# Kernel optimization log

Measured on AMD Instinct MI355X. Metric: run time of the kernel, lower is better.

## Reference

```python
import jax, jax.numpy as jnp
import numpy as np

N_VARS = 1_000_000
NB, NS, NL = 400_000, 300_000, 200_000  # binary / small-int / large-int counts
C_CLS = 16
N_CON = 500_000
E = 16_000_000
LP_SOL_COL = 8
BIAS_COL = 1
LAMBDA_MEAN, LAMBDA_MAX = 1.0, 0.1


def setup_inputs() -> dict:
    key = jax.random.key(0)
    ks = jax.random.split(key, 10)
    # disjoint variable index partitions: [0,NB) bin, [NB,NB+NS) small int,
    # [NB+NS,NB+NS+NL) large int, rest continuous (var_types==0)
    idx_bin = jnp.arange(NB, dtype=jnp.int64)
    idx_int_small = jnp.arange(NB, NB + NS, dtype=jnp.int64)
    idx_int_large = jnp.arange(NB + NS, NB + NS + NL, dtype=jnp.int64)
    var_types = jnp.concatenate([
        jnp.ones(NB, dtype=jnp.int64),                 # binary
        jnp.full((NS + NL,), 2, dtype=jnp.int64),      # integer
        jnp.zeros(N_VARS - NB - NS - NL, dtype=jnp.int64),  # continuous
    ])
    edge_indices = jnp.stack([
        jax.random.randint(ks[0], (E,), 0, N_CON, dtype=jnp.int64),
        jax.random.randint(ks[1], (E,), 0, N_VARS, dtype=jnp.int64),
    ])
    return {
        'prob_bin': jax.random.uniform(ks[2], (NB, 1), jnp.float32),
        'logits_int_small': jax.random.normal(ks[3], (NS, C_CLS), jnp.float32),
        'int_small_offsets': jax.random.normal(ks[4], (NS,), jnp.float32),
        'pred_int_large': jax.random.normal(ks[5], (NL, 1), jnp.float32),
        'edge_features': jax.random.normal(ks[6], (E, 1), jnp.float32),
        'constraint_features': jax.random.normal(ks[7], (N_CON, 8), jnp.float32),
        'variable_features': jax.random.normal(ks[8], (N_VARS, 16), jnp.float32),
        'idx_bin': idx_bin,
        'idx_int_small': idx_int_small,
        'idx_int_large': idx_int_large,
        'var_types': var_types,
        'edge_indices': edge_indices,
        'n_vars': N_VARS,
    }


def _build_x(prob_bin, logits_int_small, int_small_offsets, pred_int_large,
             variable_features, idx_bin, idx_int_small, idx_int_large,
             var_types, n_vars):
    x = jnp.zeros((n_vars,), dtype=prob_bin.dtype)
    x = x.at[idx_bin].set(prob_bin[:, 0])
    # expected value of small-int class distribution
    probs = jax.nn.softmax(logits_int_small, axis=-1)                  # [NS, C]
    class_values = jnp.arange(logits_int_small.shape[1], dtype=probs.dtype)
    expected = probs @ class_values + int_small_offsets                # [NS]
    x = x.at[idx_int_small].set(expected)
    x = x.at[idx_int_large].set(pred_int_large[:, 0])
    # continuous vars take detached LP solution values
    lp_vals = jax.lax.stop_gradient(variable_features[:, LP_SOL_COL])
    x = jnp.where(var_types == 0, lp_vals, x)
    return x


def reference(prob_bin, logits_int_small, int_small_offsets, pred_int_large,
              edge_features, constraint_features, variable_features,
              idx_bin, idx_int_small, idx_int_large, var_types,
              edge_indices, n_vars):
    x = _build_x(prob_bin, logits_int_small, int_small_offsets, pred_int_large,
                 variable_features, idx_bin, idx_int_small, idx_int_large,
                 var_types, n_vars)
    n_cons = constraint_features.shape[0]
    # sparse A @ x: gather variable values along edges, scale, scatter-add per constraint
    weighted = edge_features.reshape(-1) * x[edge_indices[1]]          # [E]
    Ax = jax.ops.segment_sum(weighted, edge_indices[0], num_segments=n_cons)
    violation = jax.nn.relu(Ax - constraint_features[:, BIAS_COL])     # [N_con]
    mean_viol = violation.mean()
    max_viol = violation.max()
    n_violated = jnp.sum(violation > 1e-6)
    penalty = LAMBDA_MEAN * mean_viol + LAMBDA_MAX * max_viol
    return penalty, mean_viol, max_viol, n_violated
```

## Files before the change

### kernel.cpp

```cpp
#include <hip/hip_runtime.h>


#define BSHIFT 14
#define BROWS  (1 << BSHIFT)
#define NBUCK_MAX 32
#define CHUNK 8192
#define ROUNDS (CHUNK / 1024)
#define BUF 128
#define THRESH 48
#define SPLIT 16

typedef int   iv4 __attribute__((ext_vector_type(4)));
typedef float fv4 __attribute__((ext_vector_type(4)));

__device__ inline unsigned pack_rec(int loc, float v) {
    unsigned f = __float_as_uint(v);
    unsigned b = (f + 0x7FFFu + ((f >> 16) & 1u)) >> 16;
    return ((unsigned)loc << 16) | b;
}


__global__ __launch_bounds__(256) void k_build_hist(
    const float* __restrict__ prob_bin, const int* __restrict__ idx_bin, int NB, int gBin,
    const float* __restrict__ logits, const float* __restrict__ offs,
    const int* __restrict__ idx_small, int NS, int gSml,
    const float* __restrict__ pred, const int* __restrict__ idx_large, int NL, int gLrg,
    const int* __restrict__ vt, const float* __restrict__ vf, int NV, int gCnt,
    const int* __restrict__ rows, int* __restrict__ counts,
    int nchunks, int E, int nbuck,
    float* __restrict__ x, float* __restrict__ acc)
{
    int blk = blockIdx.x, tid = threadIdx.x;
    if (blk == 0 && tid < 4) reinterpret_cast<unsigned*>(acc)[tid] = 0u;

    if (blk < gBin) {
        int i = blk * 256 + tid;
        if (i < NB) x[idx_bin[i]] = prob_bin[i];
        return;
    }
    blk -= gBin;
    if (blk < gSml) {
        int i = blk * 256 + tid;
        if (i < NS) {
            const fv4* lp = reinterpret_cast<const fv4*>(logits + (size_t)i * 16);
            fv4 v0 = lp[0], v1 = lp[1], v2 = lp[2], v3 = lp[3];
            float l[16] = {v0.x, v0.y, v0.z, v0.w, v1.x, v1.y, v1.z, v1.w,
                           v2.x, v2.y, v2.z, v2.w, v3.x, v3.y, v3.z, v3.w};
            float m = l[0];
#pragma unroll
            for (int j = 1; j < 16; ++j) m = fmaxf(m, l[j]);
            float s = 0.f, ws = 0.f;
#pragma unroll
            for (int j = 0; j < 16; ++j) {
                float e = expf(l[j] - m);
                s += e;
                ws += e * (float)j;
            }
            x[idx_small[i]] = ws / s + offs[i];
        }
        return;
    }
    blk -= gSml;
    if (blk < gLrg) {
        int i = blk * 256 + tid;
        if (i < NL) x[idx_large[i]] = pred[i];
        return;
    }
    blk -= gLrg;
    if (blk < gCnt) {
        int v = blk * 256 + tid;
        if (v < NV && vt[v] == 0) x[v] = vf[(size_t)v * 16 + 8];
        return;
    }
    blk -= gCnt;
    __shared__ int h[NBUCK_MAX];
    if (tid < NBUCK_MAX) h[tid] = 0;
    __syncthreads();
    int e4max = E >> 2;
    int base4 = blk * (CHUNK / 4);
#pragma unroll
    for (int k = 0; k < ROUNDS; ++k) {
        int i4 = base4 + k * 256 + tid;
        if (i4 < e4max) {
            iv4 r = reinterpret_cast<const iv4*>(rows)[i4];
            atomicAdd(&h[r.x >> BSHIFT], 1);
            atomicAdd(&h[r.y >> BSHIFT], 1);
            atomicAdd(&h[r.z >> BSHIFT], 1);
            atomicAdd(&h[r.w >> BSHIFT], 1);
        }
    }
    if (blk == 0 && tid < (E & 3))
        atomicAdd(&h[rows[(E & ~3) + tid] >> BSHIFT], 1);
    __syncthreads();
    if (tid < nbuck) counts[(size_t)tid * nchunks + blk] = h[tid];
}


__global__ void k_scanchunks(const int* __restrict__ counts, int* __restrict__ off,
                             int* __restrict__ total, int nchunks) {
    int b = blockIdx.x, lane = threadIdx.x;
    int carry = 0;
    for (int i0 = 0; i0 < nchunks; i0 += 64) {
        int i = i0 + lane;
        int v = (i < nchunks) ? counts[(size_t)b * nchunks + i] : 0;
        int orig = v;
#pragma unroll
        for (int o = 1; o < 64; o <<= 1) {
            int t = __shfl_up(v, o, 64);
            if (lane >= o) v += t;
        }
        if (i < nchunks) off[(size_t)b * nchunks + i] = carry + v - orig;
        carry += __shfl(v, 63, 64);
    }
    if (lane == 0) total[b] = carry;
}

__global__ void k_bases(const int* __restrict__ total, int* __restrict__ base, int nbuck) {
    if (blockIdx.x == 0 && threadIdx.x == 0) {
        int s = 0;
        for (int b = 0; b < nbuck; ++b) { base[b] = s; s += total[b]; }
        base[nbuck] = s;
    }
}


__global__ __launch_bounds__(256) void k_scatter3(const int* __restrict__ rows,
                                                  const int* __restrict__ cols,
                                                  const float* __restrict__ ef,
                                                  const float* __restrict__ x,
                                                  const int* __restrict__ off,
                                                  const int* __restrict__ base,
                                                  unsigned* __restrict__ recs,
                                                  int nchunks, int E, int nbuck) {
    __shared__ unsigned bufr[NBUCK_MAX][BUF];
    __shared__ int fill[NBUCK_MAX];
    __shared__ int done[NBUCK_MAX];
    __shared__ int cbase[NBUCK_MAX];

    int tid = threadIdx.x, chunk = blockIdx.x;
    if (tid < NBUCK_MAX) {
        fill[tid] = 0;
        done[tid] = 0;
        cbase[tid] = (tid < nbuck) ? base[tid] + off[(size_t)tid * nchunks + chunk] : 0;
    }
    __syncthreads();

    int e4max = E >> 2;
    int base4 = chunk * (CHUNK / 4);
    int wid = tid >> 6, lane = tid & 63;

    iv4 r, c; fv4 f;
    bool valid;
    {
        int i4 = base4 + tid;
        valid = i4 < e4max;
        if (valid) {
            r = __builtin_nontemporal_load(reinterpret_cast<const iv4*>(rows) + i4);
            c = __builtin_nontemporal_load(reinterpret_cast<const iv4*>(cols) + i4);
            f = __builtin_nontemporal_load(reinterpret_cast<const fv4*>(ef) + i4);
        }
    }

    for (int k = 0; k < ROUNDS; ++k) {
        iv4 rr = r, cc = c; fv4 ff = f;
        bool val = valid;
        if (k + 1 < ROUNDS) {
            int i4 = base4 + (k + 1) * 256 + tid;
            valid = i4 < e4max;
            if (valid) {
                r = __builtin_nontemporal_load(reinterpret_cast<const iv4*>(rows) + i4);
                c = __builtin_nontemporal_load(reinterpret_cast<const iv4*>(cols) + i4);
                f = __builtin_nontemporal_load(reinterpret_cast<const fv4*>(ef) + i4);
            }
        }
        if (val) {
            int   ra[4] = {rr.x, rr.y, rr.z, rr.w};
            int   ca[4] = {cc.x, cc.y, cc.z, cc.w};
            float fa[4] = {ff.x, ff.y, ff.z, ff.w};
#pragma unroll
            for (int j = 0; j < 4; ++j) {
                int b = ra[j] >> BSHIFT;
                unsigned rec = pack_rec(ra[j] & (BROWS - 1), fa[j] * x[ca[j]]);
                int pos = atomicAdd(&fill[b], 1);
                if (pos < BUF) bufr[b][pos] = rec;
                else recs[cbase[b] + done[b] + pos] = rec;
            }
        }
        if (k == ROUNDS - 1 && chunk == 0 && tid < (E & 3)) {
            int e = (E & ~3) + tid;
            int rrow = rows[e];
            int b = rrow >> BSHIFT;
            unsigned rec = pack_rec(rrow & (BROWS - 1), ef[e] * x[cols[e]]);
            int pos = atomicAdd(&fill[b], 1);
            if (pos < BUF) bufr[b][pos] = rec;
            else recs[cbase[b] + done[b] + pos] = rec;
        }
        __syncthreads();
        bool last = (k == ROUNDS - 1);
        for (int b = wid; b < nbuck; b += 4) {
            int fl = fill[b];
            if (fl == 0) continue;
            if (fl >= THRESH || last) {
                int n = fl < BUF ? fl : BUF;
                int g = cbase[b] + done[b];
                for (int j = lane; j < n; j += 64) recs[g + j] = bufr[b][j];
                if (lane == 0) { done[b] += fl; fill[b] = 0; }
            }
        }
        __syncthreads();
    }
}


__global__ __launch_bounds__(256) void k_accum(const unsigned* __restrict__ recs,
                                               const int* __restrict__ base,
                                               float* __restrict__ partial) {
    __shared__ float tile[BROWS];
    int tid = threadIdx.x;
    int b = blockIdx.x / SPLIT, s = blockIdx.x % SPLIT;
    for (int i = tid; i < BROWS; i += 256) tile[i] = 0.f;
    __syncthreads();
    int lo = base[b], hi = base[b + 1];
    int len = hi - lo, per = (len + SPLIT - 1) / SPLIT;
    int s0 = lo + s * per;
    int s1 = s0 + per; if (s1 > hi) s1 = hi;
    int i = s0 + tid;
    for (; i + 768 < s1; i += 1024) {
        unsigned r0 = __builtin_nontemporal_load(recs + i);
        unsigned r1 = __builtin_nontemporal_load(recs + i + 256);
        unsigned r2 = __builtin_nontemporal_load(recs + i + 512);
        unsigned r3 = __builtin_nontemporal_load(recs + i + 768);
        atomicAdd(&tile[r0 >> 16], __uint_as_float((r0 & 0xFFFFu) << 16));
        atomicAdd(&tile[r1 >> 16], __uint_as_float((r1 & 0xFFFFu) << 16));
        atomicAdd(&tile[r2 >> 16], __uint_as_float((r2 & 0xFFFFu) << 16));
        atomicAdd(&tile[r3 >> 16], __uint_as_float((r3 & 0xFFFFu) << 16));
    }
    for (; i < s1; i += 256) {
        unsigned rr = recs[i];
        atomicAdd(&tile[rr >> 16], __uint_as_float((rr & 0xFFFFu) << 16));
    }
    __syncthreads();
    float* out = partial + ((size_t)blockIdx.x << BSHIFT);
    for (int j = tid; j < BROWS; j += 256) out[j] = tile[j];
}


__global__ __launch_bounds__(256) void k_reduce_fin(const float* __restrict__ partial,
                                                    const float* __restrict__ cf,
                                                    float* __restrict__ acc,
                                                    float* __restrict__ out,
                                                    int ncon, int nblocks) {
    float lsum = 0.f, lmax = 0.f;
    unsigned lcnt = 0;
    int stride = gridDim.x * blockDim.x;
    for (int c = blockIdx.x * blockDim.x + threadIdx.x; c < ncon; c += stride) {
        int b = c >> BSHIFT, i = c & (BROWS - 1);
        const float* p = partial + (((size_t)b * SPLIT) << BSHIFT) + i;
        float v = 0.f;
#pragma unroll
        for (int s = 0; s < SPLIT; ++s)
            v += __builtin_nontemporal_load(p + ((size_t)s << BSHIFT));
        v -= cf[(size_t)c * 8 + 1];
        v = v > 0.f ? v : 0.f;
        lsum += v;
        lmax = fmaxf(lmax, v);
        lcnt += (v > 1e-6f) ? 1u : 0u;
    }
#pragma unroll
    for (int o = 32; o > 0; o >>= 1) {
        lsum += __shfl_down(lsum, o);
        lmax = fmaxf(lmax, __shfl_down(lmax, o));
        lcnt += __shfl_down(lcnt, o);
    }
    __shared__ float ssum[4];
    __shared__ float smax[4];
    __shared__ unsigned scnt[4];
    int lane = threadIdx.x & 63, wid = threadIdx.x >> 6;
    if (lane == 0) { ssum[wid] = lsum; smax[wid] = lmax; scnt[wid] = lcnt; }
    __syncthreads();
    if (threadIdx.x == 0) {
        float bs = 0.f, bm = 0.f;
        unsigned bc = 0;
        int nw = (blockDim.x + 63) >> 6;
        for (int w = 0; w < nw; ++w) { bs += ssum[w]; bm = fmaxf(bm, smax[w]); bc += scnt[w]; }
        atomicAdd(&acc[0], bs);
        atomicMax(reinterpret_cast<unsigned*>(acc) + 1, __float_as_uint(bm));
        atomicAdd(reinterpret_cast<unsigned*>(acc) + 2, bc);
        __threadfence();
        unsigned t = atomicAdd(reinterpret_cast<unsigned*>(acc) + 3, 1u);
        if (t == (unsigned)(nblocks - 1)) {
            float sum   = atomicAdd(&acc[0], 0.f);
            unsigned mb = atomicMax(reinterpret_cast<unsigned*>(acc) + 1, 0u);
            unsigned ct = atomicAdd(reinterpret_cast<unsigned*>(acc) + 2, 0u);
            float mean = sum / (float)ncon;
            float mx = __uint_as_float(mb);
            out[0] = mean + 0.1f * mx;
            out[1] = mean;
            out[2] = mx;
            out[3] = (float)ct;
        }
    }
}


__global__ void k_scatter_f(const float* __restrict__ src, const int* __restrict__ idx,
                            float* __restrict__ x, int n) {
    int i = blockIdx.x * blockDim.x + threadIdx.x;
    if (i < n) x[idx[i]] = src[i];
}

__global__ void k_edges(const float* __restrict__ ef, const int* __restrict__ rows,
                        const int* __restrict__ cols, const float* __restrict__ x,
                        float* __restrict__ Ax, int e4, int E) {
    int stride = gridDim.x * blockDim.x;
    int gid = blockIdx.x * blockDim.x + threadIdx.x;
    for (int i = gid; i < e4; i += stride) {
        fv4 f = reinterpret_cast<const fv4*>(ef)[i];
        iv4 r = reinterpret_cast<const iv4*>(rows)[i];
        iv4 c = reinterpret_cast<const iv4*>(cols)[i];
        atomicAdd(&Ax[r.x], f.x * x[c.x]);
        atomicAdd(&Ax[r.y], f.y * x[c.y]);
        atomicAdd(&Ax[r.z], f.z * x[c.z]);
        atomicAdd(&Ax[r.w], f.w * x[c.w]);
    }
    for (int e = e4 * 4 + gid; e < E; e += stride)
        atomicAdd(&Ax[rows[e]], ef[e] * x[cols[e]]);
}

__global__ void k_reduce_ax(const float* __restrict__ Ax, const float* __restrict__ cf,
                            float* __restrict__ acc, int ncon) {
    float lsum = 0.f, lmax = 0.f;
    unsigned lcnt = 0;
    int stride = gridDim.x * blockDim.x;
    for (int c = blockIdx.x * blockDim.x + threadIdx.x; c < ncon; c += stride) {
        float v = Ax[c] - cf[(size_t)c * 8 + 1];
        v = v > 0.f ? v : 0.f;
        lsum += v;
        lmax = fmaxf(lmax, v);
        lcnt += (v > 1e-6f) ? 1u : 0u;
    }
#pragma unroll
    for (int o = 32; o > 0; o >>= 1) {
        lsum += __shfl_down(lsum, o);
        lmax = fmaxf(lmax, __shfl_down(lmax, o));
        lcnt += __shfl_down(lcnt, o);
    }
    __shared__ float ssum[4];
    __shared__ float smax[4];
    __shared__ unsigned scnt[4];
    int lane = threadIdx.x & 63, wid = threadIdx.x >> 6;
    if (lane == 0) { ssum[wid] = lsum; smax[wid] = lmax; scnt[wid] = lcnt; }
    __syncthreads();
    if (threadIdx.x == 0) {
        float bs = 0.f, bm = 0.f;
        unsigned bc = 0;
        int nw = (blockDim.x + 63) >> 6;
        for (int w = 0; w < nw; ++w) { bs += ssum[w]; bm = fmaxf(bm, smax[w]); bc += scnt[w]; }
        atomicAdd(&acc[0], bs);
        atomicMax(reinterpret_cast<unsigned*>(acc) + 1, __float_as_uint(bm));
        atomicAdd(reinterpret_cast<unsigned*>(acc) + 2, bc);
    }
}

__global__ void k_final(const float* __restrict__ acc, float* __restrict__ out, int ncon) {
    if (blockIdx.x == 0 && threadIdx.x == 0) {
        float sum = acc[0];
        float mx = __uint_as_float(reinterpret_cast<const unsigned*>(acc)[1]);
        unsigned cnt = reinterpret_cast<const unsigned*>(acc)[2];
        float mean = sum / (float)ncon;
        out[0] = mean + 0.1f * mx;
        out[1] = mean;
        out[2] = mx;
        out[3] = (float)cnt;
    }
}

__global__ void k_small_int_f(const float* __restrict__ logits, const float* __restrict__ offs,
                              const int* __restrict__ idx, float* __restrict__ x, int n) {
    int i = blockIdx.x * blockDim.x + threadIdx.x;
    if (i >= n) return;
    const fv4* lp = reinterpret_cast<const fv4*>(logits + (size_t)i * 16);
    fv4 v0 = lp[0], v1 = lp[1], v2 = lp[2], v3 = lp[3];
    float l[16] = {v0.x, v0.y, v0.z, v0.w, v1.x, v1.y, v1.z, v1.w,
                   v2.x, v2.y, v2.z, v2.w, v3.x, v3.y, v3.z, v3.w};
    float m = l[0];
#pragma unroll
    for (int j = 1; j < 16; ++j) m = fmaxf(m, l[j]);
    float s = 0.f, ws = 0.f;
#pragma unroll
    for (int j = 0; j < 16; ++j) {
        float e = expf(l[j] - m);
        s += e;
        ws += e * (float)j;
    }
    x[idx[i]] = ws / s + offs[i];
}

__global__ void k_continuous_f(const int* __restrict__ vt, const float* __restrict__ vf,
                               float* __restrict__ x, int n) {
    int v = blockIdx.x * blockDim.x + threadIdx.x;
    if (v < n && vt[v] == 0) x[v] = vf[(size_t)v * 16 + 8];
}


extern "C" void kernel_launch(void* const* d_in, const int* in_sizes, int n_in,
                              void* d_out, int out_size, void* d_ws, size_t ws_size,
                              hipStream_t stream) {
    const float* prob_bin     = (const float*)d_in[0];
    const float* logits_small = (const float*)d_in[1];
    const float* offs_small   = (const float*)d_in[2];
    const float* pred_large   = (const float*)d_in[3];
    const float* edge_feat    = (const float*)d_in[4];
    const float* cons_feat    = (const float*)d_in[5];
    const float* var_feat     = (const float*)d_in[6];
    const int*   idx_bin      = (const int*)d_in[7];
    const int*   idx_small    = (const int*)d_in[8];
    const int*   idx_large    = (const int*)d_in[9];
    const int*   var_types    = (const int*)d_in[10];
    const int*   edge_indices = (const int*)d_in[11];

    const int NB    = in_sizes[0];
    const int NS    = in_sizes[2];
    const int NL    = in_sizes[3];
    const int E     = in_sizes[4];
    const int NCON  = in_sizes[5] / 8;
    const int NVARS = in_sizes[10];

    const int* rows = edge_indices;
    const int* cols = edge_indices + E;

    const int nbuck   = (NCON + BROWS - 1) >> BSHIFT;
    const int nchunks = (E + CHUNK - 1) / CHUNK;

    char* w = (char*)d_ws;
    size_t o = 0;
    auto take = [&](size_t bytes) -> char* {
        char* p = w + o;
        o = (o + bytes + 255) & ~(size_t)255;
        return p;
    };
    float*    x       = (float*)take((size_t)NVARS * 4);
    unsigned* recs    = (unsigned*)take((size_t)E * 4);
    float*    partial = (float*)take((size_t)nbuck * SPLIT * BROWS * 4);
    int*      counts  = (int*)take((size_t)nbuck * nchunks * 4);
    int*      off     = (int*)take((size_t)nbuck * nchunks * 4);
    int*      base    = (int*)take((size_t)(nbuck + 1) * 4);
    int*      total   = (int*)take((size_t)nbuck * 4);
    float*    acc     = (float*)take(16);

    bool sorted_path = (o <= ws_size) && (nbuck <= NBUCK_MAX);

    const int B = 256;

    if (sorted_path) {
        const int gBin = (NB + B - 1) / B;
        const int gSml = (NS + B - 1) / B;
        const int gLrg = (NL + B - 1) / B;
        const int gCnt = (NVARS + B - 1) / B;
        const int grid1 = gBin + gSml + gLrg + gCnt + nchunks;

        k_build_hist<<<grid1, B, 0, stream>>>(
            prob_bin, idx_bin, NB, gBin,
            logits_small, offs_small, idx_small, NS, gSml,
            pred_large, idx_large, NL, gLrg,
            var_types, var_feat, NVARS, gCnt,
            rows, counts, nchunks, E, nbuck, x, acc);
        k_scanchunks<<<nbuck, 64, 0, stream>>>(counts, off, total, nchunks);
        k_bases<<<1, 64, 0, stream>>>(total, base, nbuck);
        k_scatter3<<<nchunks, B, 0, stream>>>(rows, cols, edge_feat, x, off, base,
                                              recs, nchunks, E, nbuck);
        k_accum<<<nbuck * SPLIT, B, 0, stream>>>(recs, base, partial);
        const int rblocks = 1024;
        k_reduce_fin<<<rblocks, B, 0, stream>>>(partial, cons_feat, acc, (float*)d_out,
                                                NCON, rblocks);
    } else {
        float* accf = (float*)((char*)d_ws + (size_t)NVARS * 4);
        float* Ax   = accf + 4;
        (void)hipMemsetAsync(accf, 0, (size_t)(4 + NCON) * sizeof(float), stream);
        k_scatter_f<<<(NB + B - 1) / B, B, 0, stream>>>(prob_bin, idx_bin, x, NB);
        k_small_int_f<<<(NS + B - 1) / B, B, 0, stream>>>(logits_small, offs_small, idx_small, x, NS);
        k_scatter_f<<<(NL + B - 1) / B, B, 0, stream>>>(pred_large, idx_large, x, NL);
        k_continuous_f<<<(NVARS + B - 1) / B, B, 0, stream>>>(var_types, var_feat, x, NVARS);
        k_edges<<<2048, B, 0, stream>>>(edge_feat, rows, cols, x, Ax, E / 4, E);
        k_reduce_ax<<<1024, B, 0, stream>>>(Ax, cons_feat, accf, NCON);
        k_final<<<1, 64, 0, stream>>>(accf, (float*)d_out, NCON);
    }
}
```

Measured before the change: 313.3 us.

## Switch bucket scatter to per-wavefront strips with sync-free flushing and prefetched gathers

The histogram and scatter now work on 2048-edge strips owned by single wavefronts, so block-wide __syncthreads in the scatter loop are replaced by ballot/shuffle-driven flushes of small per-wave LDS buffers. The scatter adds a three-stage software pipeline that issues edge loads two iterations ahead and x gathers one iteration ahead. Histogram blocks are moved to the front of the fused first kernel, the scan runs 16 waves per bucket, and bucket bases are padded to multiples of four with zeroed records so accumulation can use vectorized 16-byte loads and stores. The cost is four times as many strips in counts and offsets, smaller buffers that flush to global memory more often, and added register pressure from the prefetch stages.

```diff
diff --git a/kernel.cpp b/kernel.cpp
--- a/kernel.cpp
+++ b/kernel.cpp
@@ -4,19 +4,18 @@
 #define BSHIFT 14
 #define BROWS  (1 << BSHIFT)
 #define NBUCK_MAX 32
-#define CHUNK 8192
-#define ROUNDS (CHUNK / 1024)
-#define BUF 128
-#define THRESH 48
+#define STRIP 2048
+#define NIT   (STRIP / 256)
+#define SBUF  48
+#define STHRESH 32
 #define SPLIT 16
 
 typedef int   iv4 __attribute__((ext_vector_type(4)));
 typedef float fv4 __attribute__((ext_vector_type(4)));
 
-__device__ inline unsigned pack_rec(int loc, float v) {
+__device__ inline unsigned bf16bits(float v) {
     unsigned f = __float_as_uint(v);
-    unsigned b = (f + 0x7FFFu + ((f >> 16) & 1u)) >> 16;
-    return ((unsigned)loc << 16) | b;
+    return (f + 0x7FFFu + ((f >> 16) & 1u)) >> 16;
 }
 
 
@@ -27,12 +26,37 @@
     const float* __restrict__ pred, const int* __restrict__ idx_large, int NL, int gLrg,
     const int* __restrict__ vt, const float* __restrict__ vf, int NV, int gCnt,
     const int* __restrict__ rows, int* __restrict__ counts,
-    int nchunks, int E, int nbuck,
+    int nstrips, int gHist, int E, int nbuck,
     float* __restrict__ x, float* __restrict__ acc)
 {
     int blk = blockIdx.x, tid = threadIdx.x;
     if (blk == 0 && tid < 4) reinterpret_cast<unsigned*>(acc)[tid] = 0u;
 
+    if (blk < gHist) {
+        __shared__ int h[4][NBUCK_MAX];
+        int wid = tid >> 6, lane = tid & 63;
+        int strip = blk * 4 + wid;
+        if (strip >= nstrips) return;
+        if (lane < NBUCK_MAX) h[wid][lane] = 0;
+        int e4max = E >> 2;
+        int b4 = strip * (STRIP / 4);
+#pragma unroll
+        for (int k = 0; k < NIT; ++k) {
+            int i4 = b4 + k * 64 + lane;
+            if (i4 < e4max) {
+                iv4 r = reinterpret_cast<const iv4*>(rows)[i4];
+                atomicAdd(&h[wid][r.x >> BSHIFT], 1);
+                atomicAdd(&h[wid][r.y >> BSHIFT], 1);
+                atomicAdd(&h[wid][r.z >> BSHIFT], 1);
+                atomicAdd(&h[wid][r.w >> BSHIFT], 1);
+            }
+        }
+        if (strip == 0 && lane < (E & 3))
+            atomicAdd(&h[wid][rows[(E & ~3) + lane] >> BSHIFT], 1);
+        if (lane < nbuck) counts[(size_t)lane * nstrips + strip] = h[wid][lane];
+        return;
+    }
+    blk -= gHist;
     if (blk < gBin) {
         int i = blk * 256 + tid;
         if (i < NB) x[idx_bin[i]] = prob_bin[i];
@@ -67,150 +91,162 @@
         return;
     }
     blk -= gLrg;
-    if (blk < gCnt) {
+    {
         int v = blk * 256 + tid;
         if (v < NV && vt[v] == 0) x[v] = vf[(size_t)v * 16 + 8];
-        return;
-    }
-    blk -= gCnt;
-    __shared__ int h[NBUCK_MAX];
-    if (tid < NBUCK_MAX) h[tid] = 0;
-    __syncthreads();
-    int e4max = E >> 2;
-    int base4 = blk * (CHUNK / 4);
-#pragma unroll
-    for (int k = 0; k < ROUNDS; ++k) {
-        int i4 = base4 + k * 256 + tid;
-        if (i4 < e4max) {
-            iv4 r = reinterpret_cast<const iv4*>(rows)[i4];
-            atomicAdd(&h[r.x >> BSHIFT], 1);
-            atomicAdd(&h[r.y >> BSHIFT], 1);
-            atomicAdd(&h[r.z >> BSHIFT], 1);
-            atomicAdd(&h[r.w >> BSHIFT], 1);
-        }
-    }
-    if (blk == 0 && tid < (E & 3))
-        atomicAdd(&h[rows[(E & ~3) + tid] >> BSHIFT], 1);
-    __syncthreads();
-    if (tid < nbuck) counts[(size_t)tid * nchunks + blk] = h[tid];
-}
-
-
-__global__ void k_scanchunks(const int* __restrict__ counts, int* __restrict__ off,
-                             int* __restrict__ total, int nchunks) {
-    int b = blockIdx.x, lane = threadIdx.x;
+    }
+}
+
+
+__global__ __launch_bounds__(1024) void k_scan(const int* __restrict__ counts,
+                                               int* __restrict__ off,
+                                               int* __restrict__ total, int nstrips) {
+    int b = blockIdx.x;
+    __shared__ int wtot[16];
+    __shared__ int wbase[16];
+    int tid = threadIdx.x, w = tid >> 6, lane = tid & 63;
+    int seg = (nstrips + 15) >> 4;
+    int lo = w * seg;
+    int hi = lo + seg; if (hi > nstrips) hi = nstrips;
+    const int* cb = counts + (size_t)b * nstrips;
+    int* ob = off + (size_t)b * nstrips;
     int carry = 0;
-    for (int i0 = 0; i0 < nchunks; i0 += 64) {
+    for (int i0 = lo; i0 < hi; i0 += 64) {
         int i = i0 + lane;
-        int v = (i < nchunks) ? counts[(size_t)b * nchunks + i] : 0;
+        int v = (i < hi) ? cb[i] : 0;
         int orig = v;
 #pragma unroll
         for (int o = 1; o < 64; o <<= 1) {
             int t = __shfl_up(v, o, 64);
             if (lane >= o) v += t;
         }
-        if (i < nchunks) off[(size_t)b * nchunks + i] = carry + v - orig;
+        if (i < hi) ob[i] = carry + v - orig;
         carry += __shfl(v, 63, 64);
     }
-    if (lane == 0) total[b] = carry;
-}
-
-__global__ void k_bases(const int* __restrict__ total, int* __restrict__ base, int nbuck) {
-    if (blockIdx.x == 0 && threadIdx.x == 0) {
+    if (lane == 0) wtot[w] = carry;
+    __syncthreads();
+    if (tid == 0) {
         int s = 0;
-        for (int b = 0; b < nbuck; ++b) { base[b] = s; s += total[b]; }
-        base[nbuck] = s;
-    }
-}
-
-
-__global__ __launch_bounds__(256) void k_scatter3(const int* __restrict__ rows,
+        for (int k = 0; k < 16; ++k) { wbase[k] = s; s += wtot[k]; }
+        total[b] = s;
+    }
+    __syncthreads();
+    int add = wbase[w];
+    if (add)
+        for (int i = lo + lane; i < hi; i += 64) ob[i] += add;
+}
+
+
+__global__ void k_bases(const int* __restrict__ total, int* __restrict__ base,
+                        unsigned* __restrict__ recs, int nbuck) {
+    __shared__ int sb[NBUCK_MAX + 1];
+    __shared__ int st[NBUCK_MAX];
+    int tid = threadIdx.x;
+    if (tid == 0) {
+        int s = 0;
+        for (int b = 0; b < nbuck; ++b) {
+            sb[b] = s;
+            st[b] = total[b];
+            s += (total[b] + 3) & ~3;
+        }
+        sb[nbuck] = s;
+    }
+    __syncthreads();
+    if (tid <= nbuck) base[tid] = sb[tid];
+    if (tid < nbuck) {
+        int g0 = sb[tid] + st[tid], g1 = sb[tid] + ((st[tid] + 3) & ~3);
+        for (int g = g0; g < g1; ++g) recs[g] = 0u;
+    }
+}
+
+
+__global__ __launch_bounds__(256) void k_scatter4(const int* __restrict__ rows,
                                                   const int* __restrict__ cols,
                                                   const float* __restrict__ ef,
                                                   const float* __restrict__ x,
                                                   const int* __restrict__ off,
                                                   const int* __restrict__ base,
                                                   unsigned* __restrict__ recs,
-                                                  int nchunks, int E, int nbuck) {
-    __shared__ unsigned bufr[NBUCK_MAX][BUF];
-    __shared__ int fill[NBUCK_MAX];
-    __shared__ int done[NBUCK_MAX];
-    __shared__ int cbase[NBUCK_MAX];
-
-    int tid = threadIdx.x, chunk = blockIdx.x;
-    if (tid < NBUCK_MAX) {
-        fill[tid] = 0;
-        done[tid] = 0;
-        cbase[tid] = (tid < nbuck) ? base[tid] + off[(size_t)tid * nchunks + chunk] : 0;
-    }
-    __syncthreads();
+                                                  int nstrips, int E, int nbuck) {
+    __shared__ unsigned bufr[4][NBUCK_MAX][SBUF];
+    __shared__ int      fillm[4][NBUCK_MAX];
+
+    int tid = threadIdx.x, wid = tid >> 6, lane = tid & 63;
+    int strip = blockIdx.x * 4 + wid;
+    if (strip >= nstrips) return;
+
+    unsigned (*buf)[SBUF] = bufr[wid];
+    int* fl = fillm[wid];
+    if (lane < NBUCK_MAX) fl[lane] = 0;
+
+    int cbase_r = 0, done_r = 0;
+    if (lane < nbuck) cbase_r = base[lane] + off[(size_t)lane * nstrips + strip];
 
     int e4max = E >> 2;
-    int base4 = chunk * (CHUNK / 4);
-    int wid = tid >> 6, lane = tid & 63;
-
-    iv4 r, c; fv4 f;
-    bool valid;
-    {
-        int i4 = base4 + tid;
-        valid = i4 < e4max;
-        if (valid) {
-            r = __builtin_nontemporal_load(reinterpret_cast<const iv4*>(rows) + i4);
-            c = __builtin_nontemporal_load(reinterpret_cast<const iv4*>(cols) + i4);
-            f = __builtin_nontemporal_load(reinterpret_cast<const fv4*>(ef) + i4);
-        }
-    }
-
-    for (int k = 0; k < ROUNDS; ++k) {
-        iv4 rr = r, cc = c; fv4 ff = f;
-        bool val = valid;
-        if (k + 1 < ROUNDS) {
-            int i4 = base4 + (k + 1) * 256 + tid;
-            valid = i4 < e4max;
-            if (valid) {
-                r = __builtin_nontemporal_load(reinterpret_cast<const iv4*>(rows) + i4);
-                c = __builtin_nontemporal_load(reinterpret_cast<const iv4*>(cols) + i4);
-                f = __builtin_nontemporal_load(reinterpret_cast<const fv4*>(ef) + i4);
-            }
-        }
-        if (val) {
-            int   ra[4] = {rr.x, rr.y, rr.z, rr.w};
-            int   ca[4] = {cc.x, cc.y, cc.z, cc.w};
-            float fa[4] = {ff.x, ff.y, ff.z, ff.w};
-#pragma unroll
-            for (int j = 0; j < 4; ++j) {
-                int b = ra[j] >> BSHIFT;
-                unsigned rec = pack_rec(ra[j] & (BROWS - 1), fa[j] * x[ca[j]]);
-                int pos = atomicAdd(&fill[b], 1);
-                if (pos < BUF) bufr[b][pos] = rec;
-                else recs[cbase[b] + done[b] + pos] = rec;
-            }
-        }
-        if (k == ROUNDS - 1 && chunk == 0 && tid < (E & 3)) {
-            int e = (E & ~3) + tid;
-            int rrow = rows[e];
-            int b = rrow >> BSHIFT;
-            unsigned rec = pack_rec(rrow & (BROWS - 1), ef[e] * x[cols[e]]);
-            int pos = atomicAdd(&fill[b], 1);
-            if (pos < BUF) bufr[b][pos] = rec;
-            else recs[cbase[b] + done[b] + pos] = rec;
-        }
-        __syncthreads();
-        bool last = (k == ROUNDS - 1);
-        for (int b = wid; b < nbuck; b += 4) {
-            int fl = fill[b];
-            if (fl == 0) continue;
-            if (fl >= THRESH || last) {
-                int n = fl < BUF ? fl : BUF;
-                int g = cbase[b] + done[b];
-                for (int j = lane; j < n; j += 64) recs[g + j] = bufr[b][j];
-                if (lane == 0) { done[b] += fl; fill[b] = 0; }
-            }
-        }
-        __syncthreads();
-    }
-}
-
+    int b4 = strip * (STRIP / 4);
+
+    auto PUSH1 = [&](int rr, float prod) {
+        int b = rr >> BSHIFT;
+        unsigned rec = ((unsigned)(rr & (BROWS - 1)) << 16) | bf16bits(prod);
+        int pos = atomicAdd(&fl[b], 1);
+        if (pos < SBUF) buf[b][pos] = rec;
+        else recs[__shfl(cbase_r + done_r, b) + pos] = rec;
+    };
+    auto FLUSH = [&](int thresh) {
+        int myf = (lane < nbuck) ? fl[lane] : 0;
+        unsigned long long m = __ballot(myf >= thresh);
+        while (m) {
+            int b = __ffsll((long long)m) - 1; m &= m - 1;
+            int fb = __shfl(myf, b);
+            int cur = __shfl(cbase_r + done_r, b);
+            int n = fb < SBUF ? fb : SBUF;
+            if (lane < n) recs[cur + lane] = buf[b][lane];
+            if (lane == b) { done_r += fb; fl[b] = 0; }
+        }
+    };
+
+    iv4 rs[3], cs[3]; fv4 fs[3]; bool vs[3]; fv4 gs[2];
+#define LOADS(it, s)                                                          \
+    {   int i4 = b4 + (it) * 64 + lane;                                       \
+        vs[s] = i4 < e4max;                                                   \
+        if (vs[s]) {                                                          \
+            rs[s] = __builtin_nontemporal_load(reinterpret_cast<const iv4*>(rows) + i4); \
+            cs[s] = __builtin_nontemporal_load(reinterpret_cast<const iv4*>(cols) + i4); \
+            fs[s] = __builtin_nontemporal_load(reinterpret_cast<const fv4*>(ef) + i4);   \
+        } }
+#define GATH(s, g)                                                            \
+    if (vs[s]) {                                                              \
+        gs[g].x = x[cs[s].x]; gs[g].y = x[cs[s].y];                           \
+        gs[g].z = x[cs[s].z]; gs[g].w = x[cs[s].w];                           \
+    }
+
+    LOADS(0, 0)
+    LOADS(1, 1)
+    GATH(0, 0)
+#pragma unroll
+    for (int it = 0; it < NIT; ++it) {
+        int s = it % 3, g = it & 1;
+        if (it + 2 < NIT) LOADS(it + 2, (it + 2) % 3)
+        if (it + 1 < NIT) GATH((it + 1) % 3, g ^ 1)
+        if (vs[s]) {
+            PUSH1(rs[s].x, fs[s].x * gs[g].x);
+            PUSH1(rs[s].y, fs[s].y * gs[g].y);
+            PUSH1(rs[s].z, fs[s].z * gs[g].z);
+            PUSH1(rs[s].w, fs[s].w * gs[g].w);
+        }
+        FLUSH(STHRESH);
+    }
+#undef LOADS
+#undef GATH
+    if (strip == 0 && lane < (E & 3)) {
+        int e = (E & ~3) + lane;
+        PUSH1(rows[e], ef[e] * x[cols[e]]);
+    }
+    FLUSH(1);
+}
+
+
+typedef unsigned uv4 __attribute__((ext_vector_type(4)));
 
 __global__ __launch_bounds__(256) void k_accum(const unsigned* __restrict__ recs,
                                                const int* __restrict__ base,
@@ -218,30 +254,26 @@
     __shared__ float tile[BROWS];
     int tid = threadIdx.x;
     int b = blockIdx.x / SPLIT, s = blockIdx.x % SPLIT;
-    for (int i = tid; i < BROWS; i += 256) tile[i] = 0.f;
+    fv4 z = {0.f, 0.f, 0.f, 0.f};
+    for (int i = tid; i < BROWS / 4; i += 256) reinterpret_cast<fv4*>(tile)[i] = z;
     __syncthreads();
     int lo = base[b], hi = base[b + 1];
-    int len = hi - lo, per = (len + SPLIT - 1) / SPLIT;
+    int len = hi - lo;
+    int per = ((len + SPLIT - 1) / SPLIT + 3) & ~3;
     int s0 = lo + s * per;
     int s1 = s0 + per; if (s1 > hi) s1 = hi;
-    int i = s0 + tid;
-    for (; i + 768 < s1; i += 1024) {
-        unsigned r0 = __builtin_nontemporal_load(recs + i);
-        unsigned r1 = __builtin_nontemporal_load(recs + i + 256);
-        unsigned r2 = __builtin_nontemporal_load(recs + i + 512);
-        unsigned r3 = __builtin_nontemporal_load(recs + i + 768);
-        atomicAdd(&tile[r0 >> 16], __uint_as_float((r0 & 0xFFFFu) << 16));
-        atomicAdd(&tile[r1 >> 16], __uint_as_float((r1 & 0xFFFFu) << 16));
-        atomicAdd(&tile[r2 >> 16], __uint_as_float((r2 & 0xFFFFu) << 16));
-        atomicAdd(&tile[r3 >> 16], __uint_as_float((r3 & 0xFFFFu) << 16));
-    }
-    for (; i < s1; i += 256) {
-        unsigned rr = recs[i];
-        atomicAdd(&tile[rr >> 16], __uint_as_float((rr & 0xFFFFu) << 16));
+    for (int i = s0 + (tid << 2); i + 3 < s1; i += 1024) {
+        uv4 r = __builtin_nontemporal_load(reinterpret_cast<const uv4*>(recs + i));
+        atomicAdd(&tile[(r.x >> 16) & (BROWS - 1)], __uint_as_float((r.x & 0xFFFFu) << 16));
+        atomicAdd(&tile[(r.y >> 16) & (BROWS - 1)], __uint_as_float((r.y & 0xFFFFu) << 16));
+        atomicAdd(&tile[(r.z >> 16) & (BROWS - 1)], __uint_as_float((r.z & 0xFFFFu) << 16));
+        atomicAdd(&tile[(r.w >> 16) & (BROWS - 1)], __uint_as_float((r.w & 0xFFFFu) << 16));
     }
     __syncthreads();
     float* out = partial + ((size_t)blockIdx.x << BSHIFT);
-    for (int j = tid; j < BROWS; j += 256) out[j] = tile[j];
+    for (int i = tid; i < BROWS / 4; i += 256)
+        __builtin_nontemporal_store(reinterpret_cast<const fv4*>(tile)[i],
+                                    reinterpret_cast<fv4*>(out) + i);
 }
 
 
@@ -281,8 +313,7 @@
     if (threadIdx.x == 0) {
         float bs = 0.f, bm = 0.f;
         unsigned bc = 0;
-        int nw = (blockDim.x + 63) >> 6;
-        for (int w = 0; w < nw; ++w) { bs += ssum[w]; bm = fmaxf(bm, smax[w]); bc += scnt[w]; }
+        for (int w = 0; w < 4; ++w) { bs += ssum[w]; bm = fmaxf(bm, smax[w]); bc += scnt[w]; }
         atomicAdd(&acc[0], bs);
         atomicMax(reinterpret_cast<unsigned*>(acc) + 1, __float_as_uint(bm));
         atomicAdd(reinterpret_cast<unsigned*>(acc) + 2, bc);
@@ -309,6 +340,33 @@
     if (i < n) x[idx[i]] = src[i];
 }
 
+__global__ void k_small_int_f(const float* __restrict__ logits, const float* __restrict__ offs,
+                              const int* __restrict__ idx, float* __restrict__ x, int n) {
+    int i = blockIdx.x * blockDim.x + threadIdx.x;
+    if (i >= n) return;
+    const fv4* lp = reinterpret_cast<const fv4*>(logits + (size_t)i * 16);
+    fv4 v0 = lp[0], v1 = lp[1], v2 = lp[2], v3 = lp[3];
+    float l[16] = {v0.x, v0.y, v0.z, v0.w, v1.x, v1.y, v1.z, v1.w,
+                   v2.x, v2.y, v2.z, v2.w, v3.x, v3.y, v3.z, v3.w};
+    float m = l[0];
+#pragma unroll
+    for (int j = 1; j < 16; ++j) m = fmaxf(m, l[j]);
+    float s = 0.f, ws = 0.f;
+#pragma unroll
+    for (int j = 0; j < 16; ++j) {
+        float e = expf(l[j] - m);
+        s += e;
+        ws += e * (float)j;
+    }
+    x[idx[i]] = ws / s + offs[i];
+}
+
+__global__ void k_continuous_f(const int* __restrict__ vt, const float* __restrict__ vf,
+                               float* __restrict__ x, int n) {
+    int v = blockIdx.x * blockDim.x + threadIdx.x;
+    if (v < n && vt[v] == 0) x[v] = vf[(size_t)v * 16 + 8];
+}
+
 __global__ void k_edges(const float* __restrict__ ef, const int* __restrict__ rows,
                         const int* __restrict__ cols, const float* __restrict__ x,
                         float* __restrict__ Ax, int e4, int E) {
@@ -354,8 +412,7 @@
     if (threadIdx.x == 0) {
         float bs = 0.f, bm = 0.f;
         unsigned bc = 0;
-        int nw = (blockDim.x + 63) >> 6;
-        for (int w = 0; w < nw; ++w) { bs += ssum[w]; bm = fmaxf(bm, smax[w]); bc += scnt[w]; }
+        for (int w = 0; w < 4; ++w) { bs += ssum[w]; bm = fmaxf(bm, smax[w]); bc += scnt[w]; }
         atomicAdd(&acc[0], bs);
         atomicMax(reinterpret_cast<unsigned*>(acc) + 1, __float_as_uint(bm));
         atomicAdd(reinterpret_cast<unsigned*>(acc) + 2, bc);
@@ -373,33 +430,6 @@
         out[2] = mx;
         out[3] = (float)cnt;
     }
-}
-
-__global__ void k_small_int_f(const float* __restrict__ logits, const float* __restrict__ offs,
-                              const int* __restrict__ idx, float* __restrict__ x, int n) {
-    int i = blockIdx.x * blockDim.x + threadIdx.x;
-    if (i >= n) return;
-    const fv4* lp = reinterpret_cast<const fv4*>(logits + (size_t)i * 16);
-    fv4 v0 = lp[0], v1 = lp[1], v2 = lp[2], v3 = lp[3];
-    float l[16] = {v0.x, v0.y, v0.z, v0.w, v1.x, v1.y, v1.z, v1.w,
-                   v2.x, v2.y, v2.z, v2.w, v3.x, v3.y, v3.z, v3.w};
-    float m = l[0];
-#pragma unroll
-    for (int j = 1; j < 16; ++j) m = fmaxf(m, l[j]);
-    float s = 0.f, ws = 0.f;
-#pragma unroll
-    for (int j = 0; j < 16; ++j) {
-        float e = expf(l[j] - m);
-        s += e;
-        ws += e * (float)j;
-    }
-    x[idx[i]] = ws / s + offs[i];
-}
-
-__global__ void k_continuous_f(const int* __restrict__ vt, const float* __restrict__ vf,
-                               float* __restrict__ x, int n) {
-    int v = blockIdx.x * blockDim.x + threadIdx.x;
-    if (v < n && vt[v] == 0) x[v] = vf[(size_t)v * 16 + 8];
 }
 
 
@@ -430,7 +460,7 @@
     const int* cols = edge_indices + E;
 
     const int nbuck   = (NCON + BROWS - 1) >> BSHIFT;
-    const int nchunks = (E + CHUNK - 1) / CHUNK;
+    const int nstrips = (E + STRIP - 1) / STRIP;
 
     char* w = (char*)d_ws;
     size_t o = 0;
@@ -440,10 +470,10 @@
         return p;
     };
     float*    x       = (float*)take((size_t)NVARS * 4);
-    unsigned* recs    = (unsigned*)take((size_t)E * 4);
+    unsigned* recs    = (unsigned*)take((size_t)(E + 4 * NBUCK_MAX) * 4);
     float*    partial = (float*)take((size_t)nbuck * SPLIT * BROWS * 4);
-    int*      counts  = (int*)take((size_t)nbuck * nchunks * 4);
-    int*      off     = (int*)take((size_t)nbuck * nchunks * 4);
+    int*      counts  = (int*)take((size_t)nbuck * nstrips * 4);
+    int*      off     = (int*)take((size_t)nbuck * nstrips * 4);
     int*      base    = (int*)take((size_t)(nbuck + 1) * 4);
     int*      total   = (int*)take((size_t)nbuck * 4);
     float*    acc     = (float*)take(16);
@@ -453,22 +483,23 @@
     const int B = 256;
 
     if (sorted_path) {
-        const int gBin = (NB + B - 1) / B;
-        const int gSml = (NS + B - 1) / B;
-        const int gLrg = (NL + B - 1) / B;
-        const int gCnt = (NVARS + B - 1) / B;
-        const int grid1 = gBin + gSml + gLrg + gCnt + nchunks;
+        const int gHist = (nstrips + 3) / 4;
+        const int gBin  = (NB + B - 1) / B;
+        const int gSml  = (NS + B - 1) / B;
+        const int gLrg  = (NL + B - 1) / B;
+        const int gCnt  = (NVARS + B - 1) / B;
+        const int grid1 = gHist + gBin + gSml + gLrg + gCnt;
 
         k_build_hist<<<grid1, B, 0, stream>>>(
             prob_bin, idx_bin, NB, gBin,
             logits_small, offs_small, idx_small, NS, gSml,
             pred_large, idx_large, NL, gLrg,
             var_types, var_feat, NVARS, gCnt,
-            rows, counts, nchunks, E, nbuck, x, acc);
-        k_scanchunks<<<nbuck, 64, 0, stream>>>(counts, off, total, nchunks);
-        k_bases<<<1, 64, 0, stream>>>(total, base, nbuck);
-        k_scatter3<<<nchunks, B, 0, stream>>>(rows, cols, edge_feat, x, off, base,
-                                              recs, nchunks, E, nbuck);
+            rows, counts, nstrips, gHist, E, nbuck, x, acc);
+        k_scan<<<nbuck, 1024, 0, stream>>>(counts, off, total, nstrips);
+        k_bases<<<1, 64, 0, stream>>>(total, base, recs, nbuck);
+        k_scatter4<<<(nstrips + 3) / 4, B, 0, stream>>>(rows, cols, edge_feat, x, off, base,
+                                                        recs, nstrips, E, nbuck);
         k_accum<<<nbuck * SPLIT, B, 0, stream>>>(recs, base, partial);
         const int rblocks = 1024;
         k_reduce_fin<<<rblocks, B, 0, stream>>>(partial, cons_feat, acc, (float*)d_out,
```

Result: no change. 314.1 us (+0.2%).
